# Kernel optimization log

Measured on AMD Instinct MI355X. Metric: run time of the kernel, lower is better.

The kernel has to match this reference:

```python
import jax, jax.numpy as jnp
import numpy as np

N_HIDDEN = 128
N_HEAD = 8
DIM_HEAD = N_HIDDEN // N_HEAD


def setup_inputs() -> dict:
    key = jax.random.key(0)
    ks = jax.random.split(key, 16)
    B, N, H = 2, 512, N_HIDDEN
    x = jax.random.normal(ks[0], (B, N, H), dtype=jnp.float32)
    e = jax.random.normal(ks[1], (B, N, N, H), dtype=jnp.float32)
    attention_mask = jnp.zeros((B, 1, N, N), dtype=jnp.float32)
    s = 1.0 / np.sqrt(H)
    def lin(kw, kb):
        W = jax.random.normal(kw, (H, H), dtype=jnp.float32) * s
        b = jax.random.normal(kb, (H,), dtype=jnp.float32) * s
        return W, b
    Wq, bq = lin(ks[2], ks[3])
    Wk, bk = lin(ks[4], ks[5])
    We, be = lin(ks[6], ks[7])
    Woh, boh = lin(ks[8], ks[9])
    Woe, boe = lin(ks[10], ks[11])
    return {"x": x, "e": e, "attention_mask": attention_mask,
            "Wq": Wq, "bq": bq, "Wk": Wk, "bk": bk,
            "We": We, "be": be, "Woh": Woh, "boh": boh,
            "Woe": Woe, "boe": boe}


def reference(x, e, attention_mask, Wq, bq, Wk, bk, We, be, Woh, boh, Woe, boe):
    B, N, H = x.shape
    h, dh = N_HEAD, DIM_HEAD
    # Projections -> [B, h, N, dh]
    Qx = (x @ Wq + bq).reshape(B, N, h, dh).transpose(0, 2, 1, 3)
    Kx = (x @ Wk + bk).reshape(B, N, h, dh).transpose(0, 2, 1, 3)
    Vx = Kx  # faithful to original: V_x = self.K(x)
    # Edge projection -> [B, h, N, N, dh]
    Ee = (e @ We + be).reshape(B, N, N, h, dh).transpose(0, 3, 1, 2, 4)
    # Elementwise Q*K*E biased scores: [B, h, N, N, dh]
    inter = Qx[:, :, :, None, :] * Kx[:, :, None, :, :] * Ee / np.sqrt(dh).astype(np.float32)
    scores = jax.nn.softmax(attention_mask + inter.sum(-1), axis=-1)  # [B, h, N, N]
    # Edge output: [B, N, N, H] -> Oe (dropout is identity at eval)
    e_out = inter.transpose(0, 2, 3, 1, 4).reshape(B, N, N, H) @ Woe + boe
    # Node output
    att = jnp.einsum('bhij,bhjd->bhid', scores, Vx)  # [B, h, N, dh]
    x_out = att.transpose(0, 2, 1, 3).reshape(B, N, H) @ Woh + boh
    return (x_out, e_out, scores)
```

## Files before the change

kernel.cpp:

```cpp
#include <hip/hip_runtime.h>
#include <hip/hip_bf16.h>


#define NB 2
#define NN 512
#define NHID 128
#define BQ 32

typedef __bf16 bf16x8 __attribute__((ext_vector_type(8)));
typedef __bf16 bf16x4 __attribute__((ext_vector_type(4)));
typedef float  f32x4  __attribute__((ext_vector_type(4)));

union U16 { uint4 u; bf16x8 v; };

__global__ __launch_bounds__(128)
void proj_kernel(const float* __restrict__ x,
                 const float* __restrict__ Wq, const float* __restrict__ bq,
                 const float* __restrict__ Wk, const float* __restrict__ bk,
                 float* __restrict__ Qhat, float* __restrict__ Khat)
{
    const int row = blockIdx.x;
    const int c   = threadIdx.x;
    __shared__ float xs[NHID];
    xs[c] = x[(long)row*NHID + c];
    __syncthreads();
    float q = bq[c], k = bk[c];
    #pragma unroll 8
    for (int kk = 0; kk < NHID; ++kk) {
        const float xv = xs[kk];
        q += xv * Wq[kk*NHID + c];
        k += xv * Wk[kk*NHID + c];
    }
    Qhat[(long)row*NHID + c] = q;
    Khat[(long)row*NHID + c] = k;
}

__global__ __launch_bounds__(128)
void wcvt_kernel(const float* __restrict__ We, const float* __restrict__ Woe,
                 __bf16* __restrict__ WeT, __bf16* __restrict__ WoeT)
{
    const int cb = blockIdx.x;
    const int k  = threadIdx.x;
    if (cb < NHID) {
        WeT[cb*NHID + k] = (__bf16)We[k*NHID + cb];
    } else {
        const int c = cb - NHID;
        WoeT[c*NHID + k] = (__bf16)Woe[k*NHID + c];
    }
}

__global__ __launch_bounds__(256, 3)
void mha_main(const float* __restrict__ e,
              const float* __restrict__ mask,
              const float* __restrict__ be,
              const float* __restrict__ boe,
              const float* __restrict__ Woh,
              const float* __restrict__ boh,
              const float* __restrict__ Qhat,
              const float* __restrict__ Khat,
              const __bf16* __restrict__ WeT,
              const __bf16* __restrict__ WoeT,
              float* __restrict__ xout,
              float* __restrict__ eout,
              float* __restrict__ sout)
{
    const int i   = blockIdx.x;
    const int b   = blockIdx.y;
    const int tid = threadIdx.x;
    const int w   = tid >> 6;
    const int l   = tid & 63;
    const int l15 = l & 15;
    const int lg  = l >> 4;
    const int wcol = w * 32;

    __shared__ __align__(16) __bf16 Elds[2][BQ*NHID];
    __shared__ __align__(16) __bf16 Mlds[BQ*NHID];
    __shared__ float Llog[8][NN];
    __shared__ float AttP[2][NHID];
    __shared__ float AttF[NHID];

    const long rowbi = (long)b*NN + i;
    const float* Esrc = e    + rowbi*(long)(NN*NHID);
    float*       Edst = eout + rowbi*(long)(NN*NHID);
    const float* Kb   = Khat + (long)b*NN*NHID;

    float qv[2], bev[2], boev[2];
    bf16x8 fWe[2][4], fWoe[2][4];
    #pragma unroll
    for (int ct = 0; ct < 2; ++ct) {
        const int c = wcol + ct*16 + l15;
        qv[ct]   = Qhat[rowbi*NHID + c] * 0.25f;
        bev[ct]  = be[c];
        boev[ct] = boe[c];
        #pragma unroll
        for (int ks = 0; ks < 4; ++ks) {
            const int kb = ks*32 + lg*8;
            U16 ua, ub;
            ua.u = *(const uint4*)(WeT  + c*NHID + kb);
            ub.u = *(const uint4*)(WoeT + c*NHID + kb);
            fWe[ct][ks]  = ua.v;
            fWoe[ct][ks] = ub.v;
        }
    }
    const bool selp[4] = { (0*2 + (lg>>1)) == l15, (1*2 + (lg>>1)) == l15,
                           (2*2 + (lg>>1)) == l15, (3*2 + (lg>>1)) == l15 };

    float4 rf[4];
    {
        const float4* src = (const float4*)Esrc;
        #pragma unroll
        for (int it = 0; it < 4; ++it) rf[it] = src[it*256 + tid];
        #pragma unroll
        for (int it = 0; it < 4; ++it) {
            const int L = (it*256 + tid)*4;
            const int row = L >> 7, k = L & 127;
            bf16x4 v;
            v[0]=(__bf16)rf[it].x; v[1]=(__bf16)rf[it].y;
            v[2]=(__bf16)rf[it].z; v[3]=(__bf16)rf[it].w;
            *(bf16x4*)&Elds[0][row*NHID + (k ^ ((row&7)<<3))] = v;
        }
    }

    for (int t = 0; t < 16; ++t) {
        const int cur = t & 1;
        float kreg[2][2][4];
        #pragma unroll
        for (int rt = 0; rt < 2; ++rt)
            #pragma unroll
            for (int ct = 0; ct < 2; ++ct)
                #pragma unroll
                for (int rg = 0; rg < 4; ++rg)
                    kreg[rt][ct][rg] =
                        Kb[(long)(t*BQ + rt*16 + lg*4 + rg)*NHID + wcol + ct*16 + l15];
        if (t < 15) {
            const float4* src = (const float4*)(Esrc + (long)(t+1)*(BQ*NHID));
            #pragma unroll
            for (int it = 0; it < 4; ++it) rf[it] = src[it*256 + tid];
        }
        __syncthreads();

        f32x4 acc1[2][2] = {};
        #pragma unroll
        for (int ks = 0; ks < 4; ++ks) {
            bf16x8 fa[2];
            #pragma unroll
            for (int rt = 0; rt < 2; ++rt) {
                const int row = rt*16 + l15;
                fa[rt] = *(const bf16x8*)&Elds[cur][row*NHID + ((ks*32 + lg*8) ^ ((row&7)<<3))];
            }
            #pragma unroll
            for (int rt = 0; rt < 2; ++rt)
                #pragma unroll
                for (int ct = 0; ct < 2; ++ct)
                    acc1[rt][ct] = __builtin_amdgcn_mfma_f32_16x16x32_bf16(
                        fa[rt], fWe[ct][ks], acc1[rt][ct], 0, 0, 0);
        }

        #pragma unroll
        for (int rt = 0; rt < 2; ++rt)
            #pragma unroll
            for (int ct = 0; ct < 2; ++ct) {
                const int c = wcol + ct*16 + l15;
                #pragma unroll
                for (int rg = 0; rg < 4; ++rg) {
                    const int jl = rt*16 + lg*4 + rg;
                    const float ee = acc1[rt][ct][rg] + bev[ct];
                    const float m  = ee * qv[ct] * kreg[rt][ct][rg];
                    Mlds[jl*NHID + (c ^ ((jl&7)<<3))] = (__bf16)m;
                }
            }

        if (t < 15) {
            #pragma unroll
            for (int it = 0; it < 4; ++it) {
                const int L = (it*256 + tid)*4;
                const int row = L >> 7, k = L & 127;
                bf16x4 v;
                v[0]=(__bf16)rf[it].x; v[1]=(__bf16)rf[it].y;
                v[2]=(__bf16)rf[it].z; v[3]=(__bf16)rf[it].w;
                *(bf16x4*)&Elds[1-cur][row*NHID + (k ^ ((row&7)<<3))] = v;
            }
        }
        __syncthreads();

        f32x4 acc2[2][2] = {};
        f32x4 accL[2] = {};
        #pragma unroll
        for (int ks = 0; ks < 4; ++ks) {
            bf16x8 fa[2];
            #pragma unroll
            for (int rt = 0; rt < 2; ++rt) {
                const int row = rt*16 + l15;
                fa[rt] = *(const bf16x8*)&Mlds[row*NHID + ((ks*32 + lg*8) ^ ((row&7)<<3))];
            }
            #pragma unroll
            for (int rt = 0; rt < 2; ++rt)
                #pragma unroll
                for (int ct = 0; ct < 2; ++ct)
                    acc2[rt][ct] = __builtin_amdgcn_mfma_f32_16x16x32_bf16(
                        fa[rt], fWoe[ct][ks], acc2[rt][ct], 0, 0, 0);
            if (w == 0) {
                U16 us;
                const unsigned ones = 0x3f803f80u;
                us.u.x = selp[ks] ? ones : 0u;
                us.u.y = us.u.x; us.u.z = us.u.x; us.u.w = us.u.x;
                #pragma unroll
                for (int rt = 0; rt < 2; ++rt)
                    accL[rt] = __builtin_amdgcn_mfma_f32_16x16x32_bf16(
                        fa[rt], us.v, accL[rt], 0, 0, 0);
            }
        }
        #pragma unroll
        for (int rt = 0; rt < 2; ++rt)
            #pragma unroll
            for (int ct = 0; ct < 2; ++ct) {
                const int c = wcol + ct*16 + l15;
                #pragma unroll
                for (int rg = 0; rg < 4; ++rg) {
                    const int jl = rt*16 + lg*4 + rg;
                    Edst[(long)(t*BQ + jl)*NHID + c] = acc2[rt][ct][rg] + boev[ct];
                }
            }
        if (w == 0 && l15 < 8) {
            #pragma unroll
            for (int rt = 0; rt < 2; ++rt)
                #pragma unroll
                for (int rg = 0; rg < 4; ++rg)
                    Llog[l15][t*BQ + rt*16 + lg*4 + rg] = accL[rt][rg];
        }
    }
    __syncthreads();

    const float* mrow = mask + rowbi*NN;
    #pragma unroll
    for (int hh = 0; hh < 2; ++hh) {
        const int h = w*2 + hh;
        float vb[8];
        float mx = -1e30f;
        #pragma unroll
        for (int q = 0; q < 8; ++q) {
            const int j = q*64 + l;
            const float v = Llog[h][j] + mrow[j];
            vb[q] = v; mx = fmaxf(mx, v);
        }
        #pragma unroll
        for (int mm = 1; mm < 64; mm <<= 1) mx = fmaxf(mx, __shfl_xor(mx, mm));
        float sum = 0.f;
        #pragma unroll
        for (int q = 0; q < 8; ++q) { vb[q] = __expf(vb[q] - mx); sum += vb[q]; }
        #pragma unroll
        for (int mm = 1; mm < 64; mm <<= 1) sum += __shfl_xor(sum, mm);
        const float inv = 1.f / sum;
        float* srow = sout + ((long)(b*8 + h)*NN + i)*NN;
        #pragma unroll
        for (int q = 0; q < 8; ++q) {
            const int j = q*64 + l;
            const float p = vb[q]*inv;
            Llog[h][j] = p;
            srow[j] = p;
        }
    }
    __syncthreads();

    {
        const int half = tid >> 7;
        const int c = tid & 127;
        const int h = c >> 4;
        float a0 = 0.f, a1 = 0.f, a2 = 0.f, a3 = 0.f;
        const float* kp = Kb + (long)(half*256)*NHID + c;
        const float* pp = &Llog[h][half*256];
        #pragma unroll 4
        for (int j = 0; j < 256; j += 4) {
            a0 += pp[j]   * kp[(long)(j  )*NHID];
            a1 += pp[j+1] * kp[(long)(j+1)*NHID];
            a2 += pp[j+2] * kp[(long)(j+2)*NHID];
            a3 += pp[j+3] * kp[(long)(j+3)*NHID];
        }
        AttP[half][c] = (a0 + a1) + (a2 + a3);
    }
    __syncthreads();
    if (tid < NHID) AttF[tid] = AttP[0][tid] + AttP[1][tid];
    __syncthreads();

    if (tid < NHID) {
        const int c = tid;
        float a0 = boh[c], a1 = 0.f;
        #pragma unroll 8
        for (int k = 0; k < NHID; k += 2) {
            a0 += AttF[k]   * Woh[(k  )*NHID + c];
            a1 += AttF[k+1] * Woh[(k+1)*NHID + c];
        }
        xout[rowbi*NHID + c] = a0 + a1;
    }
}

extern "C" void kernel_launch(void* const* d_in, const int* in_sizes, int n_in,
                              void* d_out, int out_size, void* d_ws, size_t ws_size,
                              hipStream_t stream) {
    const float* x    = (const float*)d_in[0];
    const float* e    = (const float*)d_in[1];
    const float* mask = (const float*)d_in[2];
    const float* Wq   = (const float*)d_in[3];
    const float* bq   = (const float*)d_in[4];
    const float* Wk   = (const float*)d_in[5];
    const float* bk   = (const float*)d_in[6];
    const float* We   = (const float*)d_in[7];
    const float* be   = (const float*)d_in[8];
    const float* Woh  = (const float*)d_in[9];
    const float* boh  = (const float*)d_in[10];
    const float* Woe  = (const float*)d_in[11];
    const float* boe  = (const float*)d_in[12];

    float*  Qhat = (float*)d_ws;
    float*  Khat = Qhat + NB*NN*NHID;
    __bf16* WeT  = (__bf16*)(Khat + NB*NN*NHID);
    __bf16* WoeT = WeT + NHID*NHID;

    float* xout = (float*)d_out;
    float* eout = xout + (long)NB*NN*NHID;
    float* sout = eout + (long)NB*NN*NN*NHID;

    proj_kernel<<<dim3(NB*NN), 128, 0, stream>>>(x, Wq, bq, Wk, bk, Qhat, Khat);
    wcvt_kernel<<<dim3(2*NHID), 128, 0, stream>>>(We, Woe, WeT, WoeT);
    mha_main<<<dim3(NN, NB), 256, 0, stream>>>(e, mask, be, boe, Woh, boh,
                                               Qhat, Khat, WeT, WoeT,
                                               xout, eout, sout);
}
```

Measured before the change: 372.8 us.

## Split softmax/attention epilogue into separate kernel to raise main-kernel occupancy

Moves the softmax and attention-times-V/output-projection epilogue out of the main edge kernel into a new kernel. Raw logits are staged through the scores output buffer in global memory instead of a 16KB LDS array. This cuts LDS use and lets launch bounds request 6 waves per SIMD instead of 3. K values are now loaded inside the product loop rather than prefetched into registers, and the large edge output uses nontemporal stores. The split adds a kernel launch plus an extra global round trip of the logits, and the later K loads may expose latency.

```diff
diff --git a/kernel.cpp b/kernel.cpp
--- a/kernel.cpp
+++ b/kernel.cpp
@@ -49,18 +49,14 @@
     }
 }
 
-__global__ __launch_bounds__(256, 3)
+__global__ __launch_bounds__(256, 6)
 void mha_main(const float* __restrict__ e,
-              const float* __restrict__ mask,
               const float* __restrict__ be,
               const float* __restrict__ boe,
-              const float* __restrict__ Woh,
-              const float* __restrict__ boh,
               const float* __restrict__ Qhat,
               const float* __restrict__ Khat,
               const __bf16* __restrict__ WeT,
               const __bf16* __restrict__ WoeT,
-              float* __restrict__ xout,
               float* __restrict__ eout,
               float* __restrict__ sout)
 {
@@ -75,9 +71,6 @@
 
     __shared__ __align__(16) __bf16 Elds[2][BQ*NHID];
     __shared__ __align__(16) __bf16 Mlds[BQ*NHID];
-    __shared__ float Llog[8][NN];
-    __shared__ float AttP[2][NHID];
-    __shared__ float AttF[NHID];
 
     const long rowbi = (long)b*NN + i;
     const float* Esrc = e    + rowbi*(long)(NN*NHID);
@@ -123,15 +116,6 @@
 
     for (int t = 0; t < 16; ++t) {
         const int cur = t & 1;
-        float kreg[2][2][4];
-        #pragma unroll
-        for (int rt = 0; rt < 2; ++rt)
-            #pragma unroll
-            for (int ct = 0; ct < 2; ++ct)
-                #pragma unroll
-                for (int rg = 0; rg < 4; ++rg)
-                    kreg[rt][ct][rg] =
-                        Kb[(long)(t*BQ + rt*16 + lg*4 + rg)*NHID + wcol + ct*16 + l15];
         if (t < 15) {
             const float4* src = (const float4*)(Esrc + (long)(t+1)*(BQ*NHID));
             #pragma unroll
@@ -164,8 +148,9 @@
                 #pragma unroll
                 for (int rg = 0; rg < 4; ++rg) {
                     const int jl = rt*16 + lg*4 + rg;
-                    const float ee = acc1[rt][ct][rg] + bev[ct];
-                    const float m  = ee * qv[ct] * kreg[rt][ct][rg];
+                    const float ee  = acc1[rt][ct][rg] + bev[ct];
+                    const float kvv = Kb[(long)(t*BQ + jl)*NHID + c];
+                    const float m   = ee * qv[ct] * kvv;
                     Mlds[jl*NHID + (c ^ ((jl&7)<<3))] = (__bf16)m;
                 }
             }
@@ -218,29 +203,53 @@
                 #pragma unroll
                 for (int rg = 0; rg < 4; ++rg) {
                     const int jl = rt*16 + lg*4 + rg;
-                    Edst[(long)(t*BQ + jl)*NHID + c] = acc2[rt][ct][rg] + boev[ct];
+                    __builtin_nontemporal_store(acc2[rt][ct][rg] + boev[ct],
+                                                &Edst[(long)(t*BQ + jl)*NHID + c]);
                 }
             }
         if (w == 0 && l15 < 8) {
+            float* lrow = sout + ((long)(b*8 + l15)*NN + i)*NN;
             #pragma unroll
             for (int rt = 0; rt < 2; ++rt)
                 #pragma unroll
                 for (int rg = 0; rg < 4; ++rg)
-                    Llog[l15][t*BQ + rt*16 + lg*4 + rg] = accL[rt][rg];
-        }
-    }
-    __syncthreads();
-
+                    lrow[t*BQ + rt*16 + lg*4 + rg] = accL[rt][rg];
+        }
+    }
+}
+
+__global__ __launch_bounds__(256)
+void epilogue_kernel(const float* __restrict__ mask,
+                     const float* __restrict__ Khat,
+                     const float* __restrict__ Woh,
+                     const float* __restrict__ boh,
+                     float* __restrict__ xout,
+                     float* __restrict__ sout)
+{
+    const int i   = blockIdx.x;
+    const int b   = blockIdx.y;
+    const int tid = threadIdx.x;
+    const int w   = tid >> 6;
+    const int l   = tid & 63;
+
+    __shared__ float Llog[8][NN];
+    __shared__ float AttP[2][NHID];
+    __shared__ float AttF[NHID];
+
+    const long rowbi = (long)b*NN + i;
     const float* mrow = mask + rowbi*NN;
+    const float* Kb   = Khat + (long)b*NN*NHID;
+
     #pragma unroll
     for (int hh = 0; hh < 2; ++hh) {
         const int h = w*2 + hh;
+        float* srow = sout + ((long)(b*8 + h)*NN + i)*NN;
         float vb[8];
         float mx = -1e30f;
         #pragma unroll
         for (int q = 0; q < 8; ++q) {
             const int j = q*64 + l;
-            const float v = Llog[h][j] + mrow[j];
+            const float v = srow[j] + mrow[j];
             vb[q] = v; mx = fmaxf(mx, v);
         }
         #pragma unroll
@@ -251,7 +260,6 @@
         #pragma unroll
         for (int mm = 1; mm < 64; mm <<= 1) sum += __shfl_xor(sum, mm);
         const float inv = 1.f / sum;
-        float* srow = sout + ((long)(b*8 + h)*NN + i)*NN;
         #pragma unroll
         for (int q = 0; q < 8; ++q) {
             const int j = q*64 + l;
@@ -322,7 +330,8 @@
 
     proj_kernel<<<dim3(NB*NN), 128, 0, stream>>>(x, Wq, bq, Wk, bk, Qhat, Khat);
     wcvt_kernel<<<dim3(2*NHID), 128, 0, stream>>>(We, Woe, WeT, WoeT);
-    mha_main<<<dim3(NN, NB), 256, 0, stream>>>(e, mask, be, boe, Woh, boh,
-                                               Qhat, Khat, WeT, WoeT,
-                                               xout, eout, sout);
-}
+    mha_main<<<dim3(NN, NB), 256, 0, stream>>>(e, be, boe, Qhat, Khat, WeT, WoeT,
+                                               eout, sout);
+    epilogue_kernel<<<dim3(NN, NB), 256, 0, stream>>>(mask, Khat, Woh, boh,
+                                                      xout, sout);
+}
```

Result: slower. 445.2 us (+19.4%).
